# Kernel optimization log

Hardware: AMD Instinct MI355X
Metric: run time of the kernel (lower is better)

The kernel has to match this reference:

```python
import jax, jax.numpy as jnp
import numpy as np

B, N, F_IN = 8, 1024, 128
H, F_OUT = 4, 64
NEG_INF = -9e15


def setup_inputs() -> dict:
    key = jax.random.key(0)
    k1, k2, k3, k4 = jax.random.split(key, 4)
    x = jax.random.normal(k1, (B, N, F_IN), dtype=jnp.float32)
    adj = jax.random.randint(k2, (B, N, N), 0, 2, dtype=jnp.int32)
    W = jax.random.normal(k3, (F_IN, H * F_OUT), dtype=jnp.float32) * 0.05
    a = jax.random.normal(k4, (H, 2 * F_OUT), dtype=jnp.float32)
    return {"x": x, "adj": adj, "W": W, "a": a}


def reference(x, adj, W, a):
    # x: [B,N,F_in], adj: [B,N,N], W: [F_in, H*F_out], a: [H, 2*F_out]
    Bs, Ns, _ = x.shape
    Hh = a.shape[0]
    Fo = a.shape[1] // 2
    h = (x @ W).reshape(Bs, Ns, Hh, Fo)            # [B,N,H,F]
    # e_{bnmh} = a . cat(h_i, h_j) = a_src . h_n + a_dst . h_m  (no O(N^2) concat)
    a_src, a_dst = a[:, :Fo], a[:, Fo:]
    e_src = jnp.einsum('bnhf,hf->bnh', h, a_src)    # [B,N,H]
    e_dst = jnp.einsum('bmhf,hf->bmh', h, a_dst)    # [B,N,H]
    e = e_src[:, :, None, :] + e_dst[:, None, :, :]  # [B,N,N,H]
    e = jax.nn.leaky_relu(e, negative_slope=0.2)
    e = jnp.where(adj[..., None] > 0, e, NEG_INF)
    attention = jax.nn.softmax(e, axis=2)           # softmax over neighbors m
    h_prime = jnp.einsum('bnmh,bmhf->bnhf', attention, h)
    return h_prime.mean(axis=2)                     # [B,N,F_out]
```

## Files before the change

kernel.cpp:

```cpp
#include <hip/hip_runtime.h>
#include <math.h>

#define Bsz 8
#define Nsz 1024
#define FIN 128
#define Hh  4
#define FO  64
#define COLS 256
#define TN  16
#define TM  32
#define BN  (Bsz*Nsz)
#define XSTR 136
#define PSTR 136
#define LOG2E  1.44269504088896340f
#define CSHIFT 17.3123404906675611f

typedef __attribute__((ext_vector_type(8))) short short8;
typedef __attribute__((ext_vector_type(4))) float f32x4;

static __device__ inline ushort f2bf(float f) {
    uint u = __float_as_uint(f);
    u += 0x7FFFu + ((u >> 16) & 1u);
    return (ushort)(u >> 16);
}
static __device__ inline float bf2f(ushort h) { return __uint_as_float(((uint)h) << 16); }

static __device__ inline float fexp2(float x) {
#if __has_builtin(__builtin_amdgcn_exp2f)
    return __builtin_amdgcn_exp2f(x);
#else
    float r; asm("v_exp_f32 %0, %1" : "=v"(r) : "v"(x));
    return r;
#endif
}

__global__ __launch_bounds__(256) void gat_prep(const float* __restrict__ W,
                                                ushort* __restrict__ Wt)
{
    const int g = blockIdx.x * 256 + threadIdx.x;
    const int n = g >> 3, kc = (g & 7) * 16;
    ushort u[16];
    #pragma unroll
    for (int i = 0; i < 16; i++) u[i] = f2bf(W[(kc + i) * COLS + n]);
    int4* dst = (int4*)(Wt + n * FIN + kc);
    dst[0] = ((int4*)u)[0];
    dst[1] = ((int4*)u)[1];
}

__global__ __launch_bounds__(256) void gat_proj(
    const float* __restrict__ x, const ushort* __restrict__ Wt,
    const float* __restrict__ a, ushort* __restrict__ h_gB,
    float* __restrict__ es_g, float* __restrict__ ed_g)
{
    __shared__ ushort xs[16 * XSTR];
    const int j    = threadIdx.x;
    const int w    = j >> 6, lane = j & 63, quad = lane >> 4, n16 = lane & 15;
    const int b    = blockIdx.x >> 6, mt16 = blockIdx.x & 63;
    const long rowbase = (long)b * Nsz + mt16 * 16;

    short8 bfr[4][4];
    #pragma unroll
    for (int kk = 0; kk < 4; kk++)
        #pragma unroll
        for (int c4 = 0; c4 < 4; c4++)
            bfr[kk][c4] = *(const short8*)(Wt + (w*64 + c4*16 + n16) * FIN + kk*32 + quad*8);

    {
        const int r = j >> 4, k0 = (j & 15) * 8;
        const float4* g4 = (const float4*)(x + (rowbase + r) * FIN + k0);
        float4 v0 = g4[0], v1 = g4[1];
        ushort u[8] = { f2bf(v0.x), f2bf(v0.y), f2bf(v0.z), f2bf(v0.w),
                        f2bf(v1.x), f2bf(v1.y), f2bf(v1.z), f2bf(v1.w) };
        *(int4*)(xs + r * XSTR + k0) = *(int4*)u;
    }
    __syncthreads();

    f32x4 acc[4];
    #pragma unroll
    for (int c4 = 0; c4 < 4; c4++)
        #pragma unroll
        for (int r = 0; r < 4; r++) acc[c4][r] = 0.f;

    #pragma unroll
    for (int kk = 0; kk < 4; kk++) {
        short8 af = *(const short8*)(xs + n16 * XSTR + kk*32 + quad*8);
        #pragma unroll
        for (int c4 = 0; c4 < 4; c4++)
            acc[c4] = __builtin_amdgcn_mfma_f32_16x16x32_bf16(af, bfr[kk][c4], acc[c4], 0, 0, 0);
    }

    const int mtile = mt16 >> 1;
    const int kbase = (mt16 & 1) * 16 + quad * 4;
    #pragma unroll
    for (int c4 = 0; c4 < 4; c4++) {
        uint2 pk;
        pk.x = (uint)f2bf(acc[c4][0]) | ((uint)f2bf(acc[c4][1]) << 16);
        pk.y = (uint)f2bf(acc[c4][2]) | ((uint)f2bf(acc[c4][3]) << 16);
        const int c = w*64 + c4*16 + n16;
        *(uint2*)(h_gB + (((long)(b*32 + mtile) * COLS + c) * 32 + kbase)) = pk;
    }

    float aS[4], aD[4];
    #pragma unroll
    for (int c4 = 0; c4 < 4; c4++) {
        aS[c4] = a[w * (2*FO) + c4*16 + n16];
        aD[c4] = a[w * (2*FO) + FO + c4*16 + n16];
    }
    #pragma unroll
    for (int reg = 0; reg < 4; reg++) {
        float ps = 0.f, pd = 0.f;
        #pragma unroll
        for (int c4 = 0; c4 < 4; c4++) {
            ps = fmaf(acc[c4][reg], aS[c4], ps);
            pd = fmaf(acc[c4][reg], aD[c4], pd);
        }
        #pragma unroll
        for (int off = 1; off < 16; off <<= 1) {
            ps += __shfl_xor(ps, off, 64);
            pd += __shfl_xor(pd, off, 64);
        }
        if (n16 == 0) {
            const long row = rowbase + quad*4 + reg;
            es_g[(long)w * BN + row] = ps * LOG2E;
            ed_g[(long)w * BN + row] = pd * LOG2E;
        }
    }
}

__global__ __launch_bounds__(512, 4) void gat_attn(
    const int* __restrict__ adj, const ushort* __restrict__ h_gB,
    const float* __restrict__ es_g, const float* __restrict__ ed_g,
    float* __restrict__ out)
{
    __shared__ ushort pT[2][2][TN * PSTR];
    __shared__ float  o_lds[2][Hh][TN][FO];
    __shared__ float  l_lds[2][TN][Hh];

    const int j    = threadIdx.x;
    const int g    = j >> 8;
    const int jg   = j & 255;
    const int w    = jg >> 6;
    const int lane = jg & 63;
    const int quad = lane >> 4, n16 = lane & 15;
    const int head = quad;
    const int mi   = n16 * 2;
    const int b    = blockIdx.x;
    const int n0   = blockIdx.y * TN;
    const long rowb = (long)b * Nsz + n0;
    const int t0   = g * 16;

    float es4[4];
    #pragma unroll
    for (int r4 = 0; r4 < 4; r4++)
        es4[r4] = es_g[(long)head * BN + rowb + w*4 + r4];

    f32x4 acc[4];
    #pragma unroll
    for (int c4 = 0; c4 < 4; c4++)
        #pragma unroll
        for (int r = 0; r < 4; r++) acc[c4][r] = 0.f;

    float l_part[4] = {0.f, 0.f, 0.f, 0.f};

    int2   ar[4];
    float2 edv;
    short8 bregA[4], bregB[4];

#define PRE_SE(t) {                                                             \
    const int m0 = (t) * TM + mi;                                               \
    _Pragma("unroll")                                                           \
    for (int r4 = 0; r4 < 4; r4++)                                              \
        ar[r4] = *(const int2*)(adj + (rowb + w*4 + r4) * (long)Nsz + m0);      \
    edv = *(const float2*)(ed_g + (long)head * BN + (long)b * Nsz + m0); }

#define PRE_B(t, brg) {                                                         \
    const ushort* hb = h_gB + (long)(b * 32 + (t)) * (COLS * TM);               \
    _Pragma("unroll")                                                           \
    for (int c4 = 0; c4 < 4; c4++)                                              \
        brg[c4] = *(const short8*)(hb + (w*64 + c4*16 + n16) * TM + quad * 8); }

#define PHASE_S(nb) {                                                           \
    _Pragma("unroll")                                                           \
    for (int r4 = 0; r4 < 4; r4++) {                                            \
        float s0 = es4[r4] + edv.x, s1 = es4[r4] + edv.y;                       \
        float u0 = fmaxf(s0, 0.2f * s0) - CSHIFT;                               \
        float u1 = fmaxf(s1, 0.2f * s1) - CSHIFT;                               \
        float e0 = fexp2(u0), e1 = fexp2(u1);                                   \
        e0 = (ar[r4].x > 0) ? e0 : 0.f;                                         \
        e1 = (ar[r4].y > 0) ? e1 : 0.f;                                         \
        uint pk;                                                                \
        asm("v_cvt_pk_bf16_f32 %0, %1, %2" : "=v"(pk) : "v"(e0), "v"(e1));      \
        *(uint*)(&pT[g][nb][(w*4 + r4) * PSTR + head * TM + mi]) = pk;          \
        l_part[r4] += __uint_as_float(pk << 16)                                 \
                    + __uint_as_float(pk & 0xFFFF0000u); } }

#define PHASE_A(cb, brg) {                                                      \
    short8 af = *(const short8*)(&pT[g][cb][n16 * PSTR + w * TM + quad * 8]);   \
    _Pragma("unroll")                                                           \
    for (int c4 = 0; c4 < 4; c4++)                                              \
        acc[c4] = __builtin_amdgcn_mfma_f32_16x16x32_bf16(af, brg[c4], acc[c4], 0, 0, 0); }

    PRE_SE(t0);
    PRE_B(t0, bregA);
    PHASE_S(0);
    PRE_SE(t0 + 1);
    PRE_B(t0 + 1, bregB);
    __syncthreads();

    for (int i = 0; i < 16; i += 2) {
        PHASE_S(1);
        if (i < 14) PRE_SE(t0 + i + 2);
        PHASE_A(0, bregA);
        if (i < 14) PRE_B(t0 + i + 2, bregA);
        __syncthreads();
        if (i < 14) PHASE_S(0);
        if (i < 14) PRE_SE(t0 + i + 3);
        PHASE_A(1, bregB);
        if (i < 14) PRE_B(t0 + i + 3, bregB);
        __syncthreads();
    }

    #pragma unroll
    for (int r4 = 0; r4 < 4; r4++) {
        float lp = l_part[r4];
        #pragma unroll
        for (int off = 1; off < 16; off <<= 1) lp += __shfl_xor(lp, off, 64);
        if (n16 == 0) l_lds[g][w*4 + r4][head] = lp;
    }
    __syncthreads();

    float rinv[4];
    #pragma unroll
    for (int reg = 0; reg < 4; reg++) {
        const int r = quad*4 + reg;
        rinv[reg] = 0.25f / (l_lds[0][r][w] + l_lds[1][r][w]);
    }
    #pragma unroll
    for (int c4 = 0; c4 < 4; c4++)
        #pragma unroll
        for (int reg = 0; reg < 4; reg++)
            o_lds[g][w][quad*4 + reg][c4*16 + n16] = acc[c4][reg] * rinv[reg];
    __syncthreads();

    {
        const int f2 = j & 63, rb = (j >> 6) & 7;
        #pragma unroll
        for (int i2 = 0; i2 < 2; i2++) {
            const int r = i2 * 8 + rb;
            float s = 0.f;
            #pragma unroll
            for (int gg = 0; gg < 2; gg++)
                #pragma unroll
                for (int ww = 0; ww < 4; ww++)
                    s += o_lds[gg][ww][r][f2];
            out[(rowb + r) * FO + f2] = s;
        }
    }
#undef PRE_SE
#undef PRE_B
#undef PHASE_S
#undef PHASE_A
}

extern "C" void kernel_launch(void* const* d_in, const int* in_sizes, int n_in,
                              void* d_out, int out_size, void* d_ws, size_t ws_size,
                              hipStream_t stream) {
    const float* x   = (const float*)d_in[0];
    const int*   adj = (const int*)d_in[1];
    const float* W   = (const float*)d_in[2];
    const float* a   = (const float*)d_in[3];
    float* out = (float*)d_out;

    ushort* Wt   = (ushort*)d_ws;
    ushort* h_gB = Wt + (size_t)COLS * FIN;
    float*  es_g = (float*)(h_gB + (size_t)BN * COLS);
    float*  ed_g = es_g + (size_t)Hh * BN;

    gat_prep<<<dim3(8),            dim3(256), 0, stream>>>(W, Wt);
    gat_proj<<<dim3(Bsz*Nsz/16),   dim3(256), 0, stream>>>(x, Wt, a, h_gB, es_g, ed_g);
    gat_attn<<<dim3(Bsz, Nsz/TN),  dim3(512), 0, stream>>>(adj, h_gB, es_g, ed_g, out);
}
```

Measured before the change: 112.2 us.

## Bit-pack adjacency and restructure attention to compute probabilities in registers

A prep pass now packs the int32 adjacency matrix into 32-bit bitmasks. The attention kernel reads these bits, stages ed values in LDS, and builds the bf16 probability fragments directly in registers rather than going through an LDS transpose buffer. The softmax denominator comes from an MFMA against a vector of ones, which removes the shuffle reductions, and the CSHIFT is folded into es. The block shrinks to 256 threads with a single group, so the split-M reduction is gone. The trade-off is an extra pass over the full 32MB adjacency in the prep kernel and more per-lane exp work, since each lane now covers all heads' columns for its row.

```diff
diff --git a/kernel.cpp b/kernel.cpp
--- a/kernel.cpp
+++ b/kernel.cpp
@@ -9,11 +9,12 @@
 #define COLS 256
 #define TN  16
 #define TM  32
+#define NT  (Nsz/TM)
 #define BN  (Bsz*Nsz)
 #define XSTR 136
-#define PSTR 136
 #define LOG2E  1.44269504088896340f
 #define CSHIFT 17.3123404906675611f
+#define NEG08C (-0.8f * CSHIFT)
 
 typedef __attribute__((ext_vector_type(8))) short short8;
 typedef __attribute__((ext_vector_type(4))) float f32x4;
@@ -23,7 +24,6 @@
     u += 0x7FFFu + ((u >> 16) & 1u);
     return (ushort)(u >> 16);
 }
-static __device__ inline float bf2f(ushort h) { return __uint_as_float(((uint)h) << 16); }
 
 static __device__ inline float fexp2(float x) {
 #if __has_builtin(__builtin_amdgcn_exp2f)
@@ -35,16 +35,33 @@
 }
 
 __global__ __launch_bounds__(256) void gat_prep(const float* __restrict__ W,
-                                                ushort* __restrict__ Wt)
+                                                ushort* __restrict__ Wt,
+                                                const int* __restrict__ adj,
+                                                uint* __restrict__ ab)
 {
-    const int g = blockIdx.x * 256 + threadIdx.x;
-    const int n = g >> 3, kc = (g & 7) * 16;
-    ushort u[16];
-    #pragma unroll
-    for (int i = 0; i < 16; i++) u[i] = f2bf(W[(kc + i) * COLS + n]);
-    int4* dst = (int4*)(Wt + n * FIN + kc);
-    dst[0] = ((int4*)u)[0];
-    dst[1] = ((int4*)u)[1];
+    if (blockIdx.x < 1024) {
+        const long g = (long)blockIdx.x * 256 + threadIdx.x;
+        const int4* src = (const int4*)(adj + g * 32);
+        uint m = 0u;
+        #pragma unroll
+        for (int i = 0; i < 8; i++) {
+            int4 v = src[i];
+            m |= (v.x > 0 ? 1u : 0u) << (i*4);
+            m |= (v.y > 0 ? 1u : 0u) << (i*4 + 1);
+            m |= (v.z > 0 ? 1u : 0u) << (i*4 + 2);
+            m |= (v.w > 0 ? 1u : 0u) << (i*4 + 3);
+        }
+        ab[g] = m;
+    } else {
+        const int g = (blockIdx.x - 1024) * 256 + threadIdx.x;
+        const int n = g >> 3, kc = (g & 7) * 16;
+        ushort u[16];
+        #pragma unroll
+        for (int i = 0; i < 16; i++) u[i] = f2bf(W[(kc + i) * COLS + n]);
+        int4* dst = (int4*)(Wt + n * FIN + kc);
+        dst[0] = ((int4*)u)[0];
+        dst[1] = ((int4*)u)[1];
+    }
 }
 
 __global__ __launch_bounds__(256) void gat_proj(
@@ -121,145 +138,123 @@
         }
         if (n16 == 0) {
             const long row = rowbase + quad*4 + reg;
-            es_g[(long)w * BN + row] = ps * LOG2E;
+            es_g[(long)w * BN + row] = ps * LOG2E - CSHIFT;
             ed_g[(long)w * BN + row] = pd * LOG2E;
         }
     }
 }
 
-__global__ __launch_bounds__(512, 4) void gat_attn(
-    const int* __restrict__ adj, const ushort* __restrict__ h_gB,
+__global__ __launch_bounds__(256, 2) void gat_attn(
+    const uint* __restrict__ ab, const ushort* __restrict__ h_gB,
     const float* __restrict__ es_g, const float* __restrict__ ed_g,
     float* __restrict__ out)
 {
-    __shared__ ushort pT[2][2][TN * PSTR];
-    __shared__ float  o_lds[2][Hh][TN][FO];
-    __shared__ float  l_lds[2][TN][Hh];
+    __shared__ __align__(16) char smem[Hh * TN * 65 * 4];
+    __shared__ uint abT[TN][36];
+    float (*edT)[Nsz]      = (float (*)[Nsz])smem;
+    float (*o_lds)[TN][65] = (float (*)[TN][65])smem;
 
     const int j    = threadIdx.x;
-    const int g    = j >> 8;
-    const int jg   = j & 255;
-    const int w    = jg >> 6;
-    const int lane = jg & 63;
-    const int quad = lane >> 4, n16 = lane & 15;
-    const int head = quad;
-    const int mi   = n16 * 2;
-    const int b    = blockIdx.x;
-    const int n0   = blockIdx.y * TN;
+    const int w    = j >> 6, lane = j & 63, quad = lane >> 4, n16 = lane & 15;
+    const int b    = blockIdx.x, n0 = blockIdx.y * TN;
     const long rowb = (long)b * Nsz + n0;
-    const int t0   = g * 16;
-
-    float es4[4];
-    #pragma unroll
-    for (int r4 = 0; r4 < 4; r4++)
-        es4[r4] = es_g[(long)head * BN + rowb + w*4 + r4];
-
-    f32x4 acc[4];
+
+    {
+        const float* src = ed_g + (long)w * BN + (long)b * Nsz + lane * 16;
+        float* dst = &edT[w][lane * 16];
+        #pragma unroll
+        for (int i = 0; i < 4; i++)
+            *(float4*)(dst + i*4) = *(const float4*)(src + i*4);
+    }
+    if (j < 128) {
+        const int r = j >> 3, c = (j & 7) * 4;
+        *(int4*)&abT[r][c] = *(const int4*)(ab + (rowb + r) * 32 + c);
+    }
+    const float esC = es_g[(long)w * BN + rowb + n16];
+    __syncthreads();
+
+    f32x4 acc[4], accl;
     #pragma unroll
     for (int c4 = 0; c4 < 4; c4++)
         #pragma unroll
         for (int r = 0; r < 4; r++) acc[c4][r] = 0.f;
-
-    float l_part[4] = {0.f, 0.f, 0.f, 0.f};
-
-    int2   ar[4];
-    float2 edv;
-    short8 bregA[4], bregB[4];
-
-#define PRE_SE(t) {                                                             \
-    const int m0 = (t) * TM + mi;                                               \
-    _Pragma("unroll")                                                           \
-    for (int r4 = 0; r4 < 4; r4++)                                              \
-        ar[r4] = *(const int2*)(adj + (rowb + w*4 + r4) * (long)Nsz + m0);      \
-    edv = *(const float2*)(ed_g + (long)head * BN + (long)b * Nsz + m0); }
-
-#define PRE_B(t, brg) {                                                         \
-    const ushort* hb = h_gB + (long)(b * 32 + (t)) * (COLS * TM);               \
+    #pragma unroll
+    for (int r = 0; r < 4; r++) accl[r] = 0.f;
+
+    short8 ones;
+    #pragma unroll
+    for (int i = 0; i < 8; i++) ones[i] = (short)0x3F80;
+
+    const ushort* hb = h_gB + (long)b * (Nsz * COLS);
+    short8 h0[4], h1[4];
+
+#define PRE_H(t, H) {                                                           \
+    const ushort* hp = hb + (long)(t) * (COLS * TM);                            \
     _Pragma("unroll")                                                           \
     for (int c4 = 0; c4 < 4; c4++)                                              \
-        brg[c4] = *(const short8*)(hb + (w*64 + c4*16 + n16) * TM + quad * 8); }
-
-#define PHASE_S(nb) {                                                           \
+        H[c4] = *(const short8*)(hp + (w*64 + c4*16 + n16) * TM + quad*8); }
+
+#define SUBT(t, HC, ABU) {                                                      \
+    f32x4 ev0 = *(const f32x4*)&edT[w][(t)*32 + quad*8];                        \
+    f32x4 ev1 = *(const f32x4*)&edT[w][(t)*32 + quad*8 + 4];                    \
+    const uint b8 = ((ABU) >> (quad*8)) & 0xffu;                                \
+    uint pk[4];                                                                 \
     _Pragma("unroll")                                                           \
-    for (int r4 = 0; r4 < 4; r4++) {                                            \
-        float s0 = es4[r4] + edv.x, s1 = es4[r4] + edv.y;                       \
-        float u0 = fmaxf(s0, 0.2f * s0) - CSHIFT;                               \
-        float u1 = fmaxf(s1, 0.2f * s1) - CSHIFT;                               \
+    for (int p2 = 0; p2 < 4; p2++) {                                            \
+        float t0 = esC + (p2 < 2 ? ev0[p2*2]     : ev1[(p2-2)*2]);              \
+        float t1 = esC + (p2 < 2 ? ev0[p2*2 + 1] : ev1[(p2-2)*2 + 1]);          \
+        float u0 = fmaxf(t0, fmaf(0.2f, t0, NEG08C));                           \
+        float u1 = fmaxf(t1, fmaf(0.2f, t1, NEG08C));                           \
         float e0 = fexp2(u0), e1 = fexp2(u1);                                   \
-        e0 = (ar[r4].x > 0) ? e0 : 0.f;                                         \
-        e1 = (ar[r4].y > 0) ? e1 : 0.f;                                         \
-        uint pk;                                                                \
-        asm("v_cvt_pk_bf16_f32 %0, %1, %2" : "=v"(pk) : "v"(e0), "v"(e1));      \
-        *(uint*)(&pT[g][nb][(w*4 + r4) * PSTR + head * TM + mi]) = pk;          \
-        l_part[r4] += __uint_as_float(pk << 16)                                 \
-                    + __uint_as_float(pk & 0xFFFF0000u); } }
-
-#define PHASE_A(cb, brg) {                                                      \
-    short8 af = *(const short8*)(&pT[g][cb][n16 * PSTR + w * TM + quad * 8]);   \
+        e0 = (b8 & (1u << (p2*2)))     ? e0 : 0.f;                              \
+        e1 = (b8 & (1u << (p2*2 + 1))) ? e1 : 0.f;                              \
+        asm("v_cvt_pk_bf16_f32 %0, %1, %2" : "=v"(pk[p2]) : "v"(e0), "v"(e1));  \
+    }                                                                           \
+    short8 af;                                                                  \
+    ((uint*)&af)[0] = pk[0]; ((uint*)&af)[1] = pk[1];                           \
+    ((uint*)&af)[2] = pk[2]; ((uint*)&af)[3] = pk[3];                           \
+    accl = __builtin_amdgcn_mfma_f32_16x16x32_bf16(af, ones, accl, 0, 0, 0);    \
     _Pragma("unroll")                                                           \
     for (int c4 = 0; c4 < 4; c4++)                                              \
-        acc[c4] = __builtin_amdgcn_mfma_f32_16x16x32_bf16(af, brg[c4], acc[c4], 0, 0, 0); }
-
-    PRE_SE(t0);
-    PRE_B(t0, bregA);
-    PHASE_S(0);
-    PRE_SE(t0 + 1);
-    PRE_B(t0 + 1, bregB);
-    __syncthreads();
-
-    for (int i = 0; i < 16; i += 2) {
-        PHASE_S(1);
-        if (i < 14) PRE_SE(t0 + i + 2);
-        PHASE_A(0, bregA);
-        if (i < 14) PRE_B(t0 + i + 2, bregA);
-        __syncthreads();
-        if (i < 14) PHASE_S(0);
-        if (i < 14) PRE_SE(t0 + i + 3);
-        PHASE_A(1, bregB);
-        if (i < 14) PRE_B(t0 + i + 3, bregB);
-        __syncthreads();
-    }
-
-    #pragma unroll
-    for (int r4 = 0; r4 < 4; r4++) {
-        float lp = l_part[r4];
-        #pragma unroll
-        for (int off = 1; off < 16; off <<= 1) lp += __shfl_xor(lp, off, 64);
-        if (n16 == 0) l_lds[g][w*4 + r4][head] = lp;
-    }
-    __syncthreads();
+        acc[c4] = __builtin_amdgcn_mfma_f32_16x16x32_bf16(af, HC[c4], acc[c4], 0, 0, 0); }
+
+    PRE_H(0, h0);
+    uint4 abq = *(const uint4*)&abT[n16][0];
+    for (int t4 = 0; t4 < NT; t4 += 4) {
+        const int tn = (t4 + 4 < NT) ? t4 + 4 : 0;
+        uint4 abn = *(const uint4*)&abT[n16][tn];
+        PRE_H(t4 + 1, h1);  SUBT(t4,     h0, abq.x);
+        PRE_H(t4 + 2, h0);  SUBT(t4 + 1, h1, abq.y);
+        PRE_H(t4 + 3, h1);  SUBT(t4 + 2, h0, abq.z);
+        if (t4 + 4 < NT) PRE_H(t4 + 4, h0);
+        SUBT(t4 + 3, h1, abq.w);
+        abq = abn;
+    }
 
     float rinv[4];
     #pragma unroll
-    for (int reg = 0; reg < 4; reg++) {
-        const int r = quad*4 + reg;
-        rinv[reg] = 0.25f / (l_lds[0][r][w] + l_lds[1][r][w]);
-    }
+    for (int reg = 0; reg < 4; reg++) rinv[reg] = 0.25f / accl[reg];
+
+    __syncthreads();
     #pragma unroll
     for (int c4 = 0; c4 < 4; c4++)
         #pragma unroll
         for (int reg = 0; reg < 4; reg++)
-            o_lds[g][w][quad*4 + reg][c4*16 + n16] = acc[c4][reg] * rinv[reg];
+            o_lds[w][quad*4 + reg][c4*16 + n16] = acc[c4][reg] * rinv[reg];
     __syncthreads();
 
     {
-        const int f2 = j & 63, rb = (j >> 6) & 7;
-        #pragma unroll
-        for (int i2 = 0; i2 < 2; i2++) {
-            const int r = i2 * 8 + rb;
-            float s = 0.f;
-            #pragma unroll
-            for (int gg = 0; gg < 2; gg++)
-                #pragma unroll
-                for (int ww = 0; ww < 4; ww++)
-                    s += o_lds[gg][ww][r][f2];
-            out[(rowb + r) * FO + f2] = s;
-        }
-    }
-#undef PRE_SE
-#undef PRE_B
-#undef PHASE_S
-#undef PHASE_A
+        const int f = j & 63, rb4 = j >> 6;
+        #pragma unroll
+        for (int i = 0; i < 4; i++) {
+            const int r = i*4 + rb4;
+            const float s = o_lds[0][r][f] + o_lds[1][r][f]
+                          + o_lds[2][r][f] + o_lds[3][r][f];
+            out[(rowb + r) * FO + f] = s;
+        }
+    }
+#undef PRE_H
+#undef SUBT
 }
 
 extern "C" void kernel_launch(void* const* d_in, const int* in_sizes, int n_in,
@@ -275,8 +270,9 @@
     ushort* h_gB = Wt + (size_t)COLS * FIN;
     float*  es_g = (float*)(h_gB + (size_t)BN * COLS);
     float*  ed_g = es_g + (size_t)Hh * BN;
-
-    gat_prep<<<dim3(8),            dim3(256), 0, stream>>>(W, Wt);
-    gat_proj<<<dim3(Bsz*Nsz/16),   dim3(256), 0, stream>>>(x, Wt, a, h_gB, es_g, ed_g);
-    gat_attn<<<dim3(Bsz, Nsz/TN),  dim3(512), 0, stream>>>(adj, h_gB, es_g, ed_g, out);
-}
+    uint*   abb  = (uint*)(ed_g + (size_t)Hh * BN);
+
+    gat_prep<<<dim3(1032),          dim3(256), 0, stream>>>(W, Wt, adj, abb);
+    gat_proj<<<dim3(Bsz*Nsz/16),    dim3(256), 0, stream>>>(x, Wt, a, h_gB, es_g, ed_g);
+    gat_attn<<<dim3(Bsz, Nsz/TN),   dim3(256), 0, stream>>>(abb, h_gB, es_g, ed_g, out);
+}
```

Result: faster. 109.6 us (-2.2%).
